# Performance work log

Hardware: AMD Instinct MI355X
Metric: run time of the kernel (lower is better)

## Reference

```python
import jax, jax.numpy as jnp
from jax import lax
import numpy as np

P = 7            # patch_size
NP = 10          # n_patches
WIN = 20         # window_size
STRIDE = 4       # window loop stride
EMB = 128        # embedding_dimension
L = WIN - P + 1  # valid-conv output side (14)
HALF = WIN // 2 - P // 2  # window start offset before clipping (7)


def _positions(H, W):
    # x outer, y inner, exactly matching the nested python loops in the source
    return np.array([(x, y) for x in range(0, H - WIN + 1, STRIDE)
                     for y in range(0, W - WIN + 1, STRIDE)], dtype=np.int32)


def _forward(images, Wp, bp, pos_emb, Wb, bb):
    B, C, H, W = images.shape
    BC = B * C
    pos = jnp.asarray(_positions(H, W))  # [Ppos, 2]

    def per_pos(p):
        x, y = p[0], p[1]
        xb0 = jnp.maximum(x - HALF, 0)          # clipped window start (x / cols)
        yb0 = jnp.maximum(y - HALF, 0)          # clipped window start (y / rows)
        winW = jnp.minimum(x - HALF + WIN, W) - xb0  # clipped window width
        winH = jnp.minimum(y - HALF + WIN, H) - yb0  # clipped window height
        # reference patch: rows y:y+P, cols x:x+P (from ORIGINAL data, as in source)
        ref = lax.dynamic_slice(images, (0, 0, y, x), (B, C, P, P)).reshape(BC, 1, P, P)
        # fixed-size window slice; upper bound never clips for our dims, lower-clip
        # handled by masking invalid candidate offsets below
        win = lax.dynamic_slice(images, (0, 0, yb0, xb0), (B, C, WIN, WIN)).reshape(BC, WIN, WIN)
        # grouped cross-correlation == torch conv2d(groups=BC) similarity
        sim = lax.conv_general_dilated(win[None], ref, (1, 1), 'VALID',
                                       feature_group_count=BC,
                                       dimension_numbers=('NCHW', 'OIHW', 'NCHW'))[0]  # [BC,L,L]
        valid = (jnp.arange(L)[:, None] <= winH - P) & (jnp.arange(L)[None, :] <= winW - P)
        sim = jnp.where(valid[None], sim, -jnp.inf)
        _, idx = lax.top_k(sim.reshape(BC, L * L), NP)  # [BC, NP]
        oy, ox = idx // L, idx % L  # row / col offsets inside the window

        def extract(w2, a, b):
            # source's meshgrid indexing yields the TRANSPOSED patch, flattened
            return lax.dynamic_slice(w2, (a, b), (P, P)).T.reshape(P * P)
        patches = jax.vmap(jax.vmap(extract, in_axes=(None, 0, 0)))(win, oy, ox)  # [BC,NP,P*P]
        # source bug kept: x_coords = row offset + x window start (and vice versa)
        return patches, oy + xb0, ox + yb0

    patches, xi, yi = jax.vmap(per_pos)(pos)  # [Ppos,BC,NP,49], [Ppos,BC,NP] int32 x2

    # NOTE: the TransformerEncoder output is discarded in the source; the actual
    # math is back_projection(projection(patches) + pos_emb).
    emb = patches.reshape(-1, B, C, NP, P * P) @ Wp + bp + pos_emb  # [Ppos,B,C,NP,EMB]
    den = (emb @ Wb + bb).reshape(-1, BC, NP, P, P)                 # [Ppos,BC,NP,P,P]

    img0 = images.reshape(BC, H, W)
    cnt0 = jnp.ones((BC, H, W), images.dtype)

    def upd(im, cn, x_i, y_i, d):
        reg = lax.dynamic_slice(im, (y_i, x_i), (P, P))
        c = lax.dynamic_slice(cn, (y_i, x_i), (P, P))
        im = lax.dynamic_update_slice(im, (reg * c + d) / (c + 1.0), (y_i, x_i))
        # source bug kept: counter incremented at transposed slice [x, y]
        ct = lax.dynamic_slice(cn, (x_i, y_i), (P, P)) + 1.0
        cn = lax.dynamic_update_slice(cn, ct, (x_i, y_i))
        return im, cn
    vupd = jax.vmap(upd)  # (b,c) planes are independent -> vectorize

    def n_step(carry, t):
        d, x_i, y_i = t
        return vupd(carry[0], carry[1], x_i, y_i, d), None

    def pos_step(carry, t):
        d, x_i, y_i = t  # d:[BC,NP,P,P]
        carry, _ = lax.scan(n_step, carry, (jnp.moveaxis(d, 1, 0), x_i.T, y_i.T))
        return carry, None

    (img, _), _ = lax.scan(pos_step, (img0, cnt0), (den, xi, yi))
    return img.reshape(B, C, H, W)


def setup_inputs() -> dict:
    key = jax.random.key(0)
    k0, k1, k2, k3 = jax.random.split(key, 4)
    B, C, H, W = 4, 8, 160, 160
    return {
        'images': jax.random.normal(k0, (B, C, H, W), jnp.float32),
        'Wp': jax.random.normal(k1, (P * P, EMB), jnp.float32) * 0.05,
        'bp': jnp.zeros((EMB,), jnp.float32),
        'pos_emb': jax.random.normal(k2, (1, NP, EMB), jnp.float32),
        'Wb': jax.random.normal(k3, (EMB, P * P), jnp.float32) * 0.05,
        'bb': jnp.zeros((P * P,), jnp.float32),
    }


def reference(images, Wp, bp, pos_emb, Wb, bb):
    return _forward(images, Wp, bp, pos_emb, Wb, bb)
```

## Files before the change

### kernel.cpp

```cpp
#include <hip/hip_runtime.h>

#define PS 7
#define NP 10
#define WIN 20
#define STR 4
#define LL 14
#define HALF 7
#define HH 160
#define WW 160
#define BCN 32
#define NX 36
#define PPOS 1296
#define EMBD 128
#define NTASK (BCN * PPOS * NP)
#define NEV (PPOS * NP)
#define CAP 512
#define NTILE 400

__global__ __launch_bounds__(256) void k_mk(const float* __restrict__ Wp,
                                            const float* __restrict__ bp,
                                            const float* __restrict__ pe,
                                            const float* __restrict__ Wb,
                                            const float* __restrict__ bb,
                                            float* __restrict__ M2,
                                            float* __restrict__ K,
                                            unsigned long long* __restrict__ MT) {
    int t = blockIdx.x * 256 + threadIdx.x;
    if (t < 49 * 49) {
        int d = t / 49, j = t % 49;
        float acc = 0.f;
        for (int e = 0; e < EMBD; ++e) acc += Wp[j * EMBD + e] * Wb[e * 49 + d];
        M2[t] = acc;
    } else if (t < 49 * 49 + NP * 49) {
        int u = t - 49 * 49;
        int n = u / 49, d = u % 49;
        float acc = bb[d];
        for (int e = 0; e < EMBD; ++e) acc += (bp[e] + pe[n * EMBD + e]) * Wb[e * 49 + d];
        K[u] = acc;
    } else if (t < 49 * 49 + NP * 49 + 256) {
        int u = t - (49 * 49 + NP * 49);
        int ey = (u >> 4) - 7, ex = (u & 15) - 7;
        int r0 = ey > 0 ? ey : 0, r1 = ey + 6 < 7 ? ey + 6 : 7;
        int c0 = ex > 0 ? ex : 0, c1 = ex + 6 < 7 ? ex + 6 : 7;
        unsigned long long m = 0ull;
        if (r0 <= r1 && c0 <= c1) {
            unsigned colp = ((1u << (c1 - c0 + 1)) - 1u) << c0;
            for (int rr = r0; rr <= r1; ++rr)
                m |= (unsigned long long)colp << (8 * rr);
        }
        MT[u] = m;
    }
}

__device__ __forceinline__ float dpp_wave_max(float x) {
    int xi = __float_as_int(x);
#define DPP_STEP(ctrl)                                                          \
    {                                                                           \
        int t_ = __builtin_amdgcn_update_dpp(xi, xi, ctrl, 0xf, 0xf, false);    \
        xi = __float_as_int(fmaxf(__int_as_float(xi), __int_as_float(t_)));     \
    }
    DPP_STEP(0x111)
    DPP_STEP(0x112)
    DPP_STEP(0x114)
    DPP_STEP(0x118)
    DPP_STEP(0x142)
    DPP_STEP(0x143)
#undef DPP_STEP
    return __int_as_float(xi);
}

__global__ __launch_bounds__(256) void k_sim(const float* __restrict__ img,
                                             unsigned* __restrict__ xy) {
    int tid  = threadIdx.x;
    int wv   = __builtin_amdgcn_readfirstlane(tid >> 6);
    int lane = tid & 63;
    int gt   = blockIdx.x * 4 + wv;
    int pos  = gt % PPOS;
    int bc   = gt / PPOS;
    int ix = pos / NX, iy = pos % NX;
    int x = ix * STR, y = iy * STR;
    int xb0 = max(x - HALF, 0), yb0 = max(y - HALF, 0);
    int jmax = x + 6 - xb0;
    int imax = y + 6 - yb0;
    const float* plane = img + bc * (HH * WW);

    float rf[49];
#pragma unroll
    for (int a = 0; a < PS; ++a)
#pragma unroll
        for (int b = 0; b < PS; ++b)
            rf[a * 7 + b] = plane[(y + a) * WW + (x + b)];

    int B = lane;
    bool bval = B < 56;
    int gr = B / 14, c = B % 14;
    int r0 = gr * 4;
    float acc[4] = {0.f, 0.f, 0.f, 0.f};
    const float* wb = plane + yb0 * WW + xb0 + c;
#pragma unroll
    for (int a = 0; a < 10; ++a) {
        int ra = min(r0 + a, 19);
        const float* rp = wb + ra * WW;
#pragma unroll
        for (int b = 0; b < 7; ++b) {
            float tap = rp[b];
#pragma unroll
            for (int k = 0; k < 4; ++k) {
                int ai = a - k;
                if (ai >= 0 && ai < 7) acc[k] += tap * rf[ai * 7 + b];
            }
        }
    }
    float v[4]; int vidx[4];
#pragma unroll
    for (int k = 0; k < 4; ++k) {
        int rr = r0 + k;
        bool ok = bval && (rr <= imax) && (c <= jmax);
        v[k] = ok ? acc[k] : -INFINITY;
        vidx[k] = rr * 14 + c;
    }

    int tbase = (bc * PPOS + pos) * NP;

    for (int n = 0; n < NP; ++n) {
        float bv = fmaxf(fmaxf(v[0], v[1]), fmaxf(v[2], v[3]));
        bv = dpp_wave_max(bv);
        float bvs = __int_as_float(__builtin_amdgcn_readlane(__float_as_int(bv), 63));
        unsigned long long ms[4];
        ms[0] = __ballot(v[0] == bvs);
        ms[1] = __ballot(v[1] == bvs);
        ms[2] = __ballot(v[2] == bvs);
        ms[3] = __ballot(v[3] == bvs);
        int best = 1 << 30, slotw = 0, lanew = 0;
#pragma unroll
        for (int s = 0; s < 4; ++s) {
            if (ms[s]) {
                int l  = __ffsll(ms[s]) - 1;
                int id = __builtin_amdgcn_readlane(vidx[s], l);
                if (id < best) { best = id; slotw = s; lanew = l; }
            }
        }
#pragma unroll
        for (int s = 0; s < 4; ++s)
            if (s == slotw && lane == lanew) v[s] = -INFINITY;

        int oy = best / 14, ox = best % 14;
        int x_i = oy + xb0;
        int y_i = ox + yb0;
        if (lane == 0) xy[tbase + n] = (unsigned)x_i | ((unsigned)y_i << 8);
    }
}

__global__ __launch_bounds__(256) void k_den(const float* __restrict__ img,
                                             const unsigned* __restrict__ xy,
                                             const float* __restrict__ M2,
                                             const float* __restrict__ Kg,
                                             float* __restrict__ pd) {
    __shared__ float xb[4][64 * 49];
    int tid  = threadIdx.x;
    int wv   = tid >> 6;
    int lane = tid & 63;
    int t = blockIdx.x * 256 + tid;
    int n = t % NP;
    int q = t / NP;
    int pos = q % PPOS;
    int bc  = q / PPOS;
    int ix = pos / NX, iy = pos % NX;
    int x = ix * STR, y = iy * STR;
    int xb0 = max(x - HALF, 0), yb0 = max(y - HALF, 0);
    unsigned u = xy[t];
    int x_i = (int)(u & 255u), y_i = (int)((u >> 8) & 255u);
    const float* src = img + bc * (HH * WW) + (yb0 + x_i - xb0) * WW + (xb0 + y_i - yb0);

    float tap[49];
#pragma unroll
    for (int j = 0; j < 49; ++j) tap[j] = src[(j % 7) * WW + (j / 7)];

    const float* kp = Kg + n * 49;
    float* xbuf = xb[wv];
    for (int d = 0; d < 49; ++d) {
        const float* mrow = M2 + d * 49;
        float a0 = 0.f, a1 = 0.f;
#pragma unroll
        for (int j = 0; j < 48; j += 2) {
            a0 = fmaf(tap[j],     mrow[j],     a0);
            a1 = fmaf(tap[j + 1], mrow[j + 1], a1);
        }
        a0 = fmaf(tap[48], mrow[48], a0);
        xbuf[lane * 49 + d] = (a0 + a1) + kp[d];
    }
    size_t base = (size_t)(blockIdx.x * 256 + wv * 64) * 49;
#pragma unroll
    for (int i = 0; i < 49; ++i)
        pd[base + i * 64 + lane] = xbuf[i * 64 + lane];
}

__global__ __launch_bounds__(256) void k_apply(const float* __restrict__ img,
                                               const unsigned* __restrict__ xy,
                                               const float* __restrict__ pd,
                                               const unsigned long long* __restrict__ mt,
                                               float* __restrict__ out) {
    __shared__ uint2 lsts[4][CAP];
    int tid  = threadIdx.x;
    int wv   = tid >> 6;
    int lane = tid & 63;
    int gt   = blockIdx.x * 4 + wv;
    int bc   = gt / NTILE;
    int tile = gt % NTILE;
    int tx0 = (tile % 20) * 8, ty0 = (tile / 20) * 8;
    int tx1 = tx0 + 7, ty1 = ty0 + 7;
    const unsigned* xs = xy + bc * NEV;
    uint2* lst = lsts[wv];

    int a0 = (tx0 <= 19) ? 0 : ((tx0 - 9) >> 2), a1 = min(35, (tx0 + 14) >> 2);
    int b0 = (ty0 <= 19) ? 0 : ((ty0 - 9) >> 2), b1 = min(35, (ty0 + 14) >> 2);
    if (a0 > b0) { int t0 = a0; a0 = b0; b0 = t0; int t1 = a1; a1 = b1; b1 = t1; }
    int lo0 = a0, lo1 = 0, len0, len1;
    if (b0 <= a1 + 1) { len0 = max(a1, b1) - lo0 + 1; len1 = 0; }
    else              { len0 = a1 - a0 + 1; lo1 = b0; len1 = b1 - b0 + 1; }
    int nU = len0 + len1;
    unsigned m = 65536u / (unsigned)nU + 1u;
    int npos = nU * nU;

    unsigned cnt = 0;
    for (int base = 0; base < npos; base += 64) {
        int k = base + lane;
        bool valid = k < npos;
        unsigned kk = valid ? (unsigned)k : 0u;
        int ki = (int)((kk * m) >> 16);
        int kj = (int)kk - ki * nU;
        int ixp = (ki < len0) ? (lo0 + ki) : (lo1 + ki - len0);
        int iyp = (kj < len0) ? (lo0 + kj) : (lo1 + kj - len0);
        int pos = ixp * NX + iyp;
        const unsigned* ep = xs + pos * NP;

        unsigned ev[NP];
#pragma unroll
        for (int n = 0; n < NP; ++n) ev[n] = ep[n];

        unsigned rel = 0;
        unsigned w0[NP], w1[NP];
#pragma unroll
        for (int n = 0; n < NP; ++n) {
            unsigned u = ev[n];
            int x_i = (int)(u & 255u);
            int y_i = (int)((u >> 8) & 255u);
            bool ih = (x_i <= tx1) && (x_i + 6 >= tx0) &&
                      (y_i <= ty1) && (y_i + 6 >= ty0);
            bool ch = (x_i <= ty1) && (x_i + 6 >= ty0) &&
                      (y_i <= tx1) && (y_i + 6 >= tx0);
            bool any = valid && (ih || ch);
            rel |= any ? (1u << n) : 0u;
            int eyH = y_i - ty0, exH = x_i - tx0;
            int eyC = x_i - ty0, exC = y_i - tx0;
            unsigned hidx = ih ? (unsigned)(((eyH + 7) << 4) | (exH + 7)) : 0u;
            unsigned cidx = ch ? (unsigned)(((eyC + 7) << 4) | (exC + 7)) : 0u;
            unsigned s8q  = ih ? (unsigned)(((7 * eyH + exH) + 48) << 2) : 0u;
            w0[n] = (unsigned)(pos * NP + n);
            w1[n] = hidx | (cidx << 8) | (s8q << 16);
        }
        int myc = __popc(rel);
        int scan = myc;
#pragma unroll
        for (int off = 1; off < 64; off <<= 1) {
            int o = __shfl_up(scan, off);
            scan += (lane >= off) ? o : 0;
        }
        int excl  = (int)cnt + scan - myc;
        int total = __shfl(scan, 63);
        int w = excl;
#pragma unroll
        for (int n = 0; n < NP; ++n) {
            if ((rel >> n) & 1u) { if (w < CAP) lst[w] = make_uint2(w0[n], w1[n]); ++w; }
        }
        cnt += (unsigned)total;
    }
    if (cnt > CAP) cnt = CAP;
    unsigned cntp = (cnt + 7u) & ~7u;
    if (cntp > CAP) cntp = CAP;
    if (lane < (int)(cntp - cnt)) lst[cnt + lane] = make_uint2(0u, 0u);
    int cntN = (int)cntp;

    int r8 = lane >> 3, c8 = lane & 7;
    int r  = ty0 + r8;
    int cc = tx0 + c8;
    float im = img[bc * (HH * WW) + r * WW + cc];
    float c  = 1.0f;
    const float* ds = pd + (size_t)bc * ((size_t)NEV * 49);
    int vOff2 = (r8 * 7 + c8) * 4 + 192;

    for (int i = 0; i < cntN; i += 8) {
        unsigned u0[8], u1[8];
        float    dv[8];
#pragma unroll
        for (int j = 0; j < 8; ++j) {
            uint2 e = lst[i + j];
            u0[j] = (unsigned)__builtin_amdgcn_readfirstlane((int)e.x);
            u1[j] = (unsigned)__builtin_amdgcn_readfirstlane((int)e.y);
        }
#pragma unroll
        for (int j = 0; j < 8; ++j) {
            int t = (int)u0[j];
            const char* dsb = (const char*)(ds + (size_t)t * 49);
            int boc = min(max(vOff2 - (int)((u1[j] >> 16) & 511u), 0), 192);
            dv[j] = *(const float*)(dsb + boc);
        }
        unsigned long long hmv[8], cmv[8];
#pragma unroll
        for (int j = 0; j < 8; ++j) {
            hmv[j] = mt[u1[j] & 255u];
            cmv[j] = mt[(u1[j] >> 8) & 255u];
        }
#pragma unroll
        for (int j = 0; j < 8; ++j) {
            float nim = fmaf(im, c, dv[j]) * __builtin_amdgcn_rcpf(c + 1.0f);
            asm("v_cndmask_b32 %0, %0, %1, %2" : "+v"(im) : "v"(nim), "s"(hmv[j]));
            float inc;
            asm("v_cndmask_b32 %0, 0, 1.0, %1" : "=v"(inc) : "s"(cmv[j]));
            c += inc;
        }
    }
    out[bc * (HH * WW) + r * WW + cc] = im;
}

extern "C" void kernel_launch(void* const* d_in, const int* in_sizes, int n_in,
                              void* d_out, int out_size, void* d_ws, size_t ws_size,
                              hipStream_t stream) {
    const float* img = (const float*)d_in[0];
    const float* Wp  = (const float*)d_in[1];
    const float* bp  = (const float*)d_in[2];
    const float* pe  = (const float*)d_in[3];
    const float* Wb  = (const float*)d_in[4];
    const float* bb  = (const float*)d_in[5];
    float* out = (float*)d_out;

    float* wsf = (float*)d_ws;
    float*              M2 = wsf;
    float*              K  = wsf + 2404;
    unsigned long long* MT = (unsigned long long*)(wsf + 2896);
    unsigned*           xy = (unsigned*)(wsf + 3408);
    float*              pd = wsf + 3408 + NTASK;

    k_mk<<<13, 256, 0, stream>>>(Wp, bp, pe, Wb, bb, M2, K, MT);
    k_sim<<<BCN * PPOS / 4, 256, 0, stream>>>(img, xy);
    k_den<<<NTASK / 256, 256, 0, stream>>>(img, xy, M2, K, pd);
    k_apply<<<BCN * NTILE / 4, 256, 0, stream>>>(img, xy, pd, MT, out);
}
```

Baseline: 287.6 us.

## Shrink k_apply blocks, swizzle block order, use DPP scan and skip empty events

k_apply now runs two waves per block instead of four and remaps block indices with an 8-way swizzle, so tiles from different planes interleave across the GPU. The wave prefix sum is replaced with a DPP-based scan plus readlane, list entries are read as 16-byte pairs, and update steps whose masks are all zero are skipped with scalar branches. The aim is to cut LDS and shuffle overhead and wasted ALU work in k_apply's hot loop, at the cost of extra branches. The new 14-bit mask on the event index is harmless because the largest index fits in 14 bits.

```diff
diff --git a/kernel.cpp b/kernel.cpp
--- a/kernel.cpp
+++ b/kernel.cpp
@@ -69,6 +69,17 @@
     return __int_as_float(xi);
 }
 
+__device__ __forceinline__ int dpp_scan_add(int x) {
+    int t;
+    t = __builtin_amdgcn_update_dpp(0, x, 0x111, 0xf, 0xf, true);  x += t;
+    t = __builtin_amdgcn_update_dpp(0, x, 0x112, 0xf, 0xf, true);  x += t;
+    t = __builtin_amdgcn_update_dpp(0, x, 0x114, 0xf, 0xf, true);  x += t;
+    t = __builtin_amdgcn_update_dpp(0, x, 0x118, 0xf, 0xf, true);  x += t;
+    t = __builtin_amdgcn_update_dpp(0, x, 0x142, 0xa, 0xf, false); x += t;
+    t = __builtin_amdgcn_update_dpp(0, x, 0x143, 0xc, 0xf, false); x += t;
+    return x;
+}
+
 __global__ __launch_bounds__(256) void k_sim(const float* __restrict__ img,
                                              unsigned* __restrict__ xy) {
     int tid  = threadIdx.x;
@@ -195,16 +206,17 @@
         pd[base + i * 64 + lane] = xbuf[i * 64 + lane];
 }
 
-__global__ __launch_bounds__(256) void k_apply(const float* __restrict__ img,
+__global__ __launch_bounds__(128) void k_apply(const float* __restrict__ img,
                                                const unsigned* __restrict__ xy,
                                                const float* __restrict__ pd,
                                                const unsigned long long* __restrict__ mt,
                                                float* __restrict__ out) {
-    __shared__ uint2 lsts[4][CAP];
+    __shared__ uint2 lsts[2][CAP];
     int tid  = threadIdx.x;
     int wv   = tid >> 6;
     int lane = tid & 63;
-    int gt   = blockIdx.x * 4 + wv;
+    int bs   = (blockIdx.x & 7) * 800 + (blockIdx.x >> 3);
+    int gt   = bs * 2 + wv;
     int bc   = gt / NTILE;
     int tile = gt % NTILE;
     int tx0 = (tile % 20) * 8, ty0 = (tile / 20) * 8;
@@ -259,15 +271,10 @@
             w0[n] = (unsigned)(pos * NP + n);
             w1[n] = hidx | (cidx << 8) | (s8q << 16);
         }
-        int myc = __popc(rel);
-        int scan = myc;
-#pragma unroll
-        for (int off = 1; off < 64; off <<= 1) {
-            int o = __shfl_up(scan, off);
-            scan += (lane >= off) ? o : 0;
-        }
+        int myc  = __popc(rel);
+        int scan = dpp_scan_add(myc);
+        int total = __builtin_amdgcn_readlane(scan, 63);
         int excl  = (int)cnt + scan - myc;
-        int total = __shfl(scan, 63);
         int w = excl;
 #pragma unroll
         for (int n = 0; n < NP; ++n) {
@@ -293,14 +300,16 @@
         unsigned u0[8], u1[8];
         float    dv[8];
 #pragma unroll
+        for (int j = 0; j < 4; ++j) {
+            uint4 e2 = *reinterpret_cast<const uint4*>(&lst[i + 2 * j]);
+            u0[2 * j]     = (unsigned)__builtin_amdgcn_readfirstlane((int)e2.x);
+            u1[2 * j]     = (unsigned)__builtin_amdgcn_readfirstlane((int)e2.y);
+            u0[2 * j + 1] = (unsigned)__builtin_amdgcn_readfirstlane((int)e2.z);
+            u1[2 * j + 1] = (unsigned)__builtin_amdgcn_readfirstlane((int)e2.w);
+        }
+#pragma unroll
         for (int j = 0; j < 8; ++j) {
-            uint2 e = lst[i + j];
-            u0[j] = (unsigned)__builtin_amdgcn_readfirstlane((int)e.x);
-            u1[j] = (unsigned)__builtin_amdgcn_readfirstlane((int)e.y);
-        }
-#pragma unroll
-        for (int j = 0; j < 8; ++j) {
-            int t = (int)u0[j];
+            int t = (int)(u0[j] & 16383u);
             const char* dsb = (const char*)(ds + (size_t)t * 49);
             int boc = min(max(vOff2 - (int)((u1[j] >> 16) & 511u), 0), 192);
             dv[j] = *(const float*)(dsb + boc);
@@ -313,11 +322,15 @@
         }
 #pragma unroll
         for (int j = 0; j < 8; ++j) {
-            float nim = fmaf(im, c, dv[j]) * __builtin_amdgcn_rcpf(c + 1.0f);
-            asm("v_cndmask_b32 %0, %0, %1, %2" : "+v"(im) : "v"(nim), "s"(hmv[j]));
-            float inc;
-            asm("v_cndmask_b32 %0, 0, 1.0, %1" : "=v"(inc) : "s"(cmv[j]));
-            c += inc;
+            if (hmv[j] != 0ull) {
+                float nim = fmaf(im, c, dv[j]) * __builtin_amdgcn_rcpf(c + 1.0f);
+                asm("v_cndmask_b32 %0, %0, %1, %2" : "+v"(im) : "v"(nim), "s"(hmv[j]));
+            }
+            if (cmv[j] != 0ull) {
+                float inc;
+                asm("v_cndmask_b32 %0, 0, 1.0, %1" : "=v"(inc) : "s"(cmv[j]));
+                c += inc;
+            }
         }
     }
     out[bc * (HH * WW) + r * WW + cc] = im;
@@ -344,5 +357,5 @@
     k_mk<<<13, 256, 0, stream>>>(Wp, bp, pe, Wb, bb, M2, K, MT);
     k_sim<<<BCN * PPOS / 4, 256, 0, stream>>>(img, xy);
     k_den<<<NTASK / 256, 256, 0, stream>>>(img, xy, M2, K, pd);
-    k_apply<<<BCN * NTILE / 4, 256, 0, stream>>>(img, xy, pd, MT, out);
-}
+    k_apply<<<BCN * NTILE / 2, 128, 0, stream>>>(img, xy, pd, MT, out);
+}
```

Measured after the change: 298.1 us. 3.6% more time.
